# Performance work log

Hardware: AMD Instinct MI355X
Metric: run time of the kernel (lower is better)

Reference implementation:

```python
import jax, jax.numpy as jnp
import numpy as np

B, S, DIM = 4, 4096, 1024
H, HD = 16, 64  # n_heads, head_dim = dim // n_heads
UMV = 20.0      # unified_max_value (init kwarg)


def setup_inputs() -> dict:
    key = jax.random.key(0)
    kx, kw = jax.random.split(key)
    x = jax.random.normal(kx, (B, S, DIM), dtype=jnp.float32)
    # qkv_proj: Linear(dim, 3*dim). Small weight scale + positive bias keeps
    # attention scores inside the keep-window [0, 2*UMV] so denominators are safe.
    W_qkv = jax.random.normal(kw, (DIM, 3 * DIM), dtype=jnp.float32) * 0.02
    b_qkv = jnp.full((3 * DIM,), 0.5, dtype=jnp.float32)
    return {"x": x, "W_qkv": W_qkv, "b_qkv": b_qkv}


def reference(x, W_qkv, b_qkv):
    Bb, Ss, _ = x.shape
    qkv = x @ W_qkv + b_qkv                      # [B,S,3*dim]
    qkv = qkv.reshape(Bb, Ss, H, 3 * HD)          # [B,S,H,3*hd]
    Q, K, V = jnp.split(qkv, 3, axis=-1)          # each [B,S,H,hd]
    # matmul(Q, K.transpose(-2,-1)) on [B,S,H,hd]: contract head_dim -> [B,S,H,H]
    s = jnp.einsum('bshd,bsgd->bshg', Q, K) - UMV
    e = jnp.exp(s)
    mask = (s > UMV) | (s < -UMV)                 # keep only s in [-UMV, UMV]
    e = jnp.where(mask, 0.0, e)
    denom = jnp.sum(e, axis=-1, keepdims=True)
    p = e / denom                                  # [B,S,H,H]
    out = jnp.einsum('bshg,bsgd->bshd', p, V)      # [B,S,H,hd]
    return out
```

## Files before the change

### kernel.cpp

```cpp
#include <hip/hip_runtime.h>

typedef _Float16 v8h __attribute__((ext_vector_type(8)));
typedef _Float16 v4h __attribute__((ext_vector_type(4)));
typedef float v4f __attribute__((ext_vector_type(4)));

__device__ __forceinline__ void gl16(const void* g, void* l) {
    __builtin_amdgcn_global_load_lds(
        (const __attribute__((address_space(1))) unsigned int*)g,
        (__attribute__((address_space(3))) unsigned int*)l, 16, 0, 0);
}

__global__ __launch_bounds__(256) void k_cvt_x(const float* __restrict__ x,
                                               _Float16* __restrict__ x16) {
    int i = (blockIdx.x * 256 + threadIdx.x) * 8;
    float4 a = *(const float4*)(x + i);
    float4 b = *(const float4*)(x + i + 4);
    v8h h;
    h[0] = (_Float16)a.x; h[1] = (_Float16)a.y; h[2] = (_Float16)a.z; h[3] = (_Float16)a.w;
    h[4] = (_Float16)b.x; h[5] = (_Float16)b.y; h[6] = (_Float16)b.z; h[7] = (_Float16)b.w;
    *(v8h*)(x16 + i) = h;
}

__global__ __launch_bounds__(256) void k_cvt_w(const float* __restrict__ W,
                                               _Float16* __restrict__ Wt) {
    __shared__ float T[64][68];
    int k0 = (blockIdx.x & 15) * 64;
    int n0 = (blockIdx.x >> 4) * 64;
    int t = threadIdx.x;
    int tr = t >> 4;
    int tc = t & 15;
#pragma unroll
    for (int rr = 0; rr < 4; rr++) {
        int kk = rr * 16 + tr;
        float4 v = *(const float4*)(W + (size_t)(k0 + kk) * 3072 + n0 + tc * 4);
        T[kk][tc * 4 + 0] = v.x; T[kk][tc * 4 + 1] = v.y;
        T[kk][tc * 4 + 2] = v.z; T[kk][tc * 4 + 3] = v.w;
    }
    __syncthreads();
#pragma unroll
    for (int ww = 0; ww < 4; ww++) {
        int nn = ww * 16 + tr;
        v4h h;
#pragma unroll
        for (int i = 0; i < 4; i++) h[i] = (_Float16)T[tc * 4 + i][nn];
        *(v4h*)(Wt + (size_t)(n0 + nn) * 1024 + k0 + tc * 4) = h;
    }
}

__global__ __launch_bounds__(256) void k_gemm(const _Float16* __restrict__ A,
                                              const _Float16* __restrict__ Bt,
                                              const float* __restrict__ bias,
                                              float* __restrict__ C) {
    __shared__ __align__(16) _Float16 As[128 * 32];
    __shared__ __align__(16) _Float16 Bs[128 * 32];
    int bm = blockIdx.x & 127;
    int bn = blockIdx.x >> 7;
    int m0 = bm * 128, n0 = bn * 128;
    int tid = threadIdx.x;
    int w = tid >> 6, lane = tid & 63;
    int quad = lane >> 4, l15 = lane & 15;
    int wm = (w & 1) * 64, wn = (w >> 1) * 64;

    int mc1 = w * 16 + (lane >> 2);
    int mc2 = (w + 4) * 16 + (lane >> 2);
    int k8 = (lane & 3) * 8;
    const _Float16* aS1 = A + (size_t)(m0 + mc1) * 1024 + k8;
    const _Float16* aS2 = A + (size_t)(m0 + mc2) * 1024 + k8;
    const _Float16* bS1 = Bt + (size_t)(n0 + mc1) * 1024 + k8;
    const _Float16* bS2 = Bt + (size_t)(n0 + mc2) * 1024 + k8;
    _Float16* lA1 = &As[w * 512];
    _Float16* lA2 = &As[(w + 4) * 512];
    _Float16* lB1 = &Bs[w * 512];
    _Float16* lB2 = &Bs[(w + 4) * 512];

    v4f acc[4][4] = {};

    for (int kt = 0; kt < 1024; kt += 32) {
        __syncthreads();
        gl16(aS1 + kt, lA1);
        gl16(aS2 + kt, lA2);
        gl16(bS1 + kt, lB1);
        gl16(bS2 + kt, lB2);
        __syncthreads();
        v8h af[4], bf[4];
#pragma unroll
        for (int mi = 0; mi < 4; mi++)
            af[mi] = *(const v8h*)&As[(wm + mi * 16 + l15) * 32 + quad * 8];
#pragma unroll
        for (int ni = 0; ni < 4; ni++)
            bf[ni] = *(const v8h*)&Bs[(wn + ni * 16 + l15) * 32 + quad * 8];
#pragma unroll
        for (int mi = 0; mi < 4; mi++)
#pragma unroll
            for (int ni = 0; ni < 4; ni++)
                acc[mi][ni] = __builtin_amdgcn_mfma_f32_16x16x32_f16(af[mi], bf[ni], acc[mi][ni], 0, 0, 0);
    }

#pragma unroll
    for (int ni = 0; ni < 4; ni++) {
        int n = n0 + wn + ni * 16 + l15;
        float bv = bias[n];
#pragma unroll
        for (int mi = 0; mi < 4; mi++) {
            int mbase = m0 + wm + mi * 16 + quad * 4;
#pragma unroll
            for (int r = 0; r < 4; r++)
                C[(size_t)(mbase + r) * 3072 + n] = acc[mi][ni][r] + bv;
        }
    }
}

__global__ __launch_bounds__(256) void k_attn(const float* __restrict__ qkv,
                                              float* __restrict__ out) {
    __shared__ __align__(16) float lds[4 * 3408];
    int tid = threadIdx.x;
    int w = tid >> 6, lane = tid & 63;
    int pos = blockIdx.x * 4 + w;
    float* L = &lds[w * 3408];
    float* P = L + 3136;
    const float* src = qkv + (size_t)pos * 3072;

#pragma unroll
    for (int ii = 0; ii < 12; ii++) {
        int e = (ii * 64 + lane) * 4;
        float4 v = *(const float4*)(src + e);
        int h = e / 192, r = e % 192;
        *(float4*)(L + h * 196 + r) = v;
    }
    __syncthreads();

    {
        int h = lane & 15, quad = lane >> 4;
        const float* Qr = L + h * 196;
        const float* Kr0 = L + (quad * 4 + 0) * 196 + 64;
        const float* Kr1 = L + (quad * 4 + 1) * 196 + 64;
        const float* Kr2 = L + (quad * 4 + 2) * 196 + 64;
        const float* Kr3 = L + (quad * 4 + 3) * 196 + 64;
        float a0 = 0.f, a1 = 0.f, a2 = 0.f, a3 = 0.f;
#pragma unroll
        for (int d4 = 0; d4 < 16; d4++) {
            float4 q = *(const float4*)(Qr + d4 * 4);
            float4 k0 = *(const float4*)(Kr0 + d4 * 4);
            float4 k1 = *(const float4*)(Kr1 + d4 * 4);
            float4 k2 = *(const float4*)(Kr2 + d4 * 4);
            float4 k3 = *(const float4*)(Kr3 + d4 * 4);
            a0 += q.x * k0.x + q.y * k0.y + q.z * k0.z + q.w * k0.w;
            a1 += q.x * k1.x + q.y * k1.y + q.z * k1.z + q.w * k1.w;
            a2 += q.x * k2.x + q.y * k2.y + q.z * k2.z + q.w * k2.w;
            a3 += q.x * k3.x + q.y * k3.y + q.z * k3.z + q.w * k3.w;
        }
        float s0 = a0 - 20.0f, s1 = a1 - 20.0f, s2 = a2 - 20.0f, s3 = a3 - 20.0f;
        float e0 = (s0 > 20.0f || s0 < -20.0f) ? 0.0f : expf(s0);
        float e1 = (s1 > 20.0f || s1 < -20.0f) ? 0.0f : expf(s1);
        float e2 = (s2 > 20.0f || s2 < -20.0f) ? 0.0f : expf(s2);
        float e3 = (s3 > 20.0f || s3 < -20.0f) ? 0.0f : expf(s3);
        float part = e0 + e1 + e2 + e3;
        part += __shfl_xor(part, 16, 64);
        part += __shfl_xor(part, 32, 64);
        float inv = 1.0f / part;
        P[h * 17 + quad * 4 + 0] = e0 * inv;
        P[h * 17 + quad * 4 + 1] = e1 * inv;
        P[h * 17 + quad * 4 + 2] = e2 * inv;
        P[h * 17 + quad * 4 + 3] = e3 * inv;
    }
    __syncthreads();

    {
        int h2 = lane >> 2, db = (lane & 3) * 16;
        float o[16];
#pragma unroll
        for (int i = 0; i < 16; i++) o[i] = 0.f;
#pragma unroll
        for (int g = 0; g < 16; g++) {
            float p = P[h2 * 17 + g];
            const float* Vr = L + g * 196 + 128 + db;
#pragma unroll
            for (int d4 = 0; d4 < 4; d4++) {
                float4 v = *(const float4*)(Vr + d4 * 4);
                o[d4 * 4 + 0] += p * v.x;
                o[d4 * 4 + 1] += p * v.y;
                o[d4 * 4 + 2] += p * v.z;
                o[d4 * 4 + 3] += p * v.w;
            }
        }
        float* dst = out + (size_t)pos * 1024 + h2 * 64 + db;
#pragma unroll
        for (int d4 = 0; d4 < 4; d4++) {
            float4 v;
            v.x = o[d4 * 4 + 0]; v.y = o[d4 * 4 + 1];
            v.z = o[d4 * 4 + 2]; v.w = o[d4 * 4 + 3];
            *(float4*)(dst + d4 * 4) = v;
        }
    }
}

extern "C" void kernel_launch(void* const* d_in, const int* in_sizes, int n_in,
                              void* d_out, int out_size, void* d_ws, size_t ws_size,
                              hipStream_t stream) {
    (void)in_sizes; (void)n_in; (void)out_size; (void)ws_size;
    const float* x    = (const float*)d_in[0];
    const float* Wq   = (const float*)d_in[1];
    const float* bq   = (const float*)d_in[2];
    float* out = (float*)d_out;

    char* ws = (char*)d_ws;
    _Float16* x16  = (_Float16*)ws;
    _Float16* wt16 = (_Float16*)(ws + 33554432);
    float*    qkv  = (float*)(ws + 33554432 + 6291456);

    k_cvt_x<<<8192, 256, 0, stream>>>(x, x16);
    k_cvt_w<<<768, 256, 0, stream>>>(Wq, wt16);
    k_gemm<<<3072, 256, 0, stream>>>(x16, wt16, bq, qkv);
    k_attn<<<4096, 256, 0, stream>>>(qkv, out);
}
```

Baseline: 315.7 us.

## Store QKV intermediate in fp16 and use fdot2 in attention

```diff
diff --git a/kernel.cpp b/kernel.cpp
--- a/kernel.cpp
+++ b/kernel.cpp
@@ -2,6 +2,7 @@
 
 typedef _Float16 v8h __attribute__((ext_vector_type(8)));
 typedef _Float16 v4h __attribute__((ext_vector_type(4)));
+typedef _Float16 v2h __attribute__((ext_vector_type(2)));
 typedef float v4f __attribute__((ext_vector_type(4)));
 
 __device__ __forceinline__ void gl16(const void* g, void* l) {
@@ -50,7 +51,7 @@
 __global__ __launch_bounds__(256) void k_gemm(const _Float16* __restrict__ A,
                                               const _Float16* __restrict__ Bt,
                                               const float* __restrict__ bias,
-                                              float* __restrict__ C) {
+                                              _Float16* __restrict__ C) {
     __shared__ __align__(16) _Float16 As[128 * 32];
     __shared__ __align__(16) _Float16 Bs[128 * 32];
     int bm = blockIdx.x & 127;
@@ -105,63 +106,58 @@
             int mbase = m0 + wm + mi * 16 + quad * 4;
 #pragma unroll
             for (int r = 0; r < 4; r++)
-                C[(size_t)(mbase + r) * 3072 + n] = acc[mi][ni][r] + bv;
-        }
-    }
-}
-
-__global__ __launch_bounds__(256) void k_attn(const float* __restrict__ qkv,
+                C[(size_t)(mbase + r) * 3072 + n] = (_Float16)(acc[mi][ni][r] + bv);
+        }
+    }
+}
+
+__global__ __launch_bounds__(256) void k_attn(const _Float16* __restrict__ qkv,
                                               float* __restrict__ out) {
-    __shared__ __align__(16) float lds[4 * 3408];
+    __shared__ __align__(16) _Float16 Lh[4][16 * 200];
+    __shared__ float Pb[4][16 * 17];
     int tid = threadIdx.x;
     int w = tid >> 6, lane = tid & 63;
     int pos = blockIdx.x * 4 + w;
-    float* L = &lds[w * 3408];
-    float* P = L + 3136;
-    const float* src = qkv + (size_t)pos * 3072;
-
-#pragma unroll
-    for (int ii = 0; ii < 12; ii++) {
-        int e = (ii * 64 + lane) * 4;
-        float4 v = *(const float4*)(src + e);
+    _Float16* L = Lh[w];
+    float* P = Pb[w];
+    const _Float16* src = qkv + (size_t)pos * 3072;
+
+#pragma unroll
+    for (int ii = 0; ii < 6; ii++) {
+        int e = (ii * 64 + lane) * 8;
+        v8h v = *(const v8h*)(src + e);
         int h = e / 192, r = e % 192;
-        *(float4*)(L + h * 196 + r) = v;
+        *(v8h*)(L + h * 200 + r) = v;
     }
     __syncthreads();
 
     {
         int h = lane & 15, quad = lane >> 4;
-        const float* Qr = L + h * 196;
-        const float* Kr0 = L + (quad * 4 + 0) * 196 + 64;
-        const float* Kr1 = L + (quad * 4 + 1) * 196 + 64;
-        const float* Kr2 = L + (quad * 4 + 2) * 196 + 64;
-        const float* Kr3 = L + (quad * 4 + 3) * 196 + 64;
-        float a0 = 0.f, a1 = 0.f, a2 = 0.f, a3 = 0.f;
-#pragma unroll
-        for (int d4 = 0; d4 < 16; d4++) {
-            float4 q = *(const float4*)(Qr + d4 * 4);
-            float4 k0 = *(const float4*)(Kr0 + d4 * 4);
-            float4 k1 = *(const float4*)(Kr1 + d4 * 4);
-            float4 k2 = *(const float4*)(Kr2 + d4 * 4);
-            float4 k3 = *(const float4*)(Kr3 + d4 * 4);
-            a0 += q.x * k0.x + q.y * k0.y + q.z * k0.z + q.w * k0.w;
-            a1 += q.x * k1.x + q.y * k1.y + q.z * k1.z + q.w * k1.w;
-            a2 += q.x * k2.x + q.y * k2.y + q.z * k2.z + q.w * k2.w;
-            a3 += q.x * k3.x + q.y * k3.y + q.z * k3.z + q.w * k3.w;
-        }
-        float s0 = a0 - 20.0f, s1 = a1 - 20.0f, s2 = a2 - 20.0f, s3 = a3 - 20.0f;
-        float e0 = (s0 > 20.0f || s0 < -20.0f) ? 0.0f : expf(s0);
-        float e1 = (s1 > 20.0f || s1 < -20.0f) ? 0.0f : expf(s1);
-        float e2 = (s2 > 20.0f || s2 < -20.0f) ? 0.0f : expf(s2);
-        float e3 = (s3 > 20.0f || s3 < -20.0f) ? 0.0f : expf(s3);
-        float part = e0 + e1 + e2 + e3;
+        const _Float16* Qr = L + h * 200;
+        v8h q[8];
+#pragma unroll
+        for (int d = 0; d < 8; d++) q[d] = *(const v8h*)(Qr + d * 8);
+        float e4[4];
+#pragma unroll
+        for (int c = 0; c < 4; c++) {
+            const _Float16* Kr = L + (quad * 4 + c) * 200 + 64;
+            float a = 0.f;
+#pragma unroll
+            for (int d = 0; d < 8; d++) {
+                v8h k = *(const v8h*)(Kr + d * 8);
+#pragma unroll
+                for (int j = 0; j < 4; j++)
+                    a = __builtin_amdgcn_fdot2(((v2h*)&q[d])[j], ((v2h*)&k)[j], a, false);
+            }
+            float s = a - 20.0f;
+            e4[c] = (s > 20.0f || s < -20.0f) ? 0.0f : __expf(s);
+        }
+        float part = e4[0] + e4[1] + e4[2] + e4[3];
         part += __shfl_xor(part, 16, 64);
         part += __shfl_xor(part, 32, 64);
         float inv = 1.0f / part;
-        P[h * 17 + quad * 4 + 0] = e0 * inv;
-        P[h * 17 + quad * 4 + 1] = e1 * inv;
-        P[h * 17 + quad * 4 + 2] = e2 * inv;
-        P[h * 17 + quad * 4 + 3] = e3 * inv;
+#pragma unroll
+        for (int c = 0; c < 4; c++) P[h * 17 + quad * 4 + c] = e4[c] * inv;
     }
     __syncthreads();
 
@@ -173,14 +169,13 @@
 #pragma unroll
         for (int g = 0; g < 16; g++) {
             float p = P[h2 * 17 + g];
-            const float* Vr = L + g * 196 + 128 + db;
-#pragma unroll
-            for (int d4 = 0; d4 < 4; d4++) {
-                float4 v = *(const float4*)(Vr + d4 * 4);
-                o[d4 * 4 + 0] += p * v.x;
-                o[d4 * 4 + 1] += p * v.y;
-                o[d4 * 4 + 2] += p * v.z;
-                o[d4 * 4 + 3] += p * v.w;
+            const _Float16* Vr = L + g * 200 + 128 + db;
+            v8h v0 = *(const v8h*)(Vr);
+            v8h v1 = *(const v8h*)(Vr + 8);
+#pragma unroll
+            for (int i = 0; i < 8; i++) {
+                o[i]     += p * (float)v0[i];
+                o[8 + i] += p * (float)v1[i];
             }
         }
         float* dst = out + (size_t)pos * 1024 + h2 * 64 + db;
@@ -198,18 +193,18 @@
                               void* d_out, int out_size, void* d_ws, size_t ws_size,
                               hipStream_t stream) {
     (void)in_sizes; (void)n_in; (void)out_size; (void)ws_size;
-    const float* x    = (const float*)d_in[0];
-    const float* Wq   = (const float*)d_in[1];
-    const float* bq   = (const float*)d_in[2];
+    const float* x  = (const float*)d_in[0];
+    const float* Wq = (const float*)d_in[1];
+    const float* bq = (const float*)d_in[2];
     float* out = (float*)d_out;
 
     char* ws = (char*)d_ws;
-    _Float16* x16  = (_Float16*)ws;
-    _Float16* wt16 = (_Float16*)(ws + 33554432);
-    float*    qkv  = (float*)(ws + 33554432 + 6291456);
+    _Float16* x16   = (_Float16*)ws;
+    _Float16* wt16  = (_Float16*)(ws + (32u << 20));
+    _Float16* qkv16 = (_Float16*)(ws + (38u << 20));
 
     k_cvt_x<<<8192, 256, 0, stream>>>(x, x16);
     k_cvt_w<<<768, 256, 0, stream>>>(Wq, wt16);
-    k_gemm<<<3072, 256, 0, stream>>>(x16, wt16, bq, qkv);
-    k_attn<<<4096, 256, 0, stream>>>(qkv, out);
-}
+    k_gemm<<<3072, 256, 0, stream>>>(x16, wt16, bq, qkv16);
+    k_attn<<<4096, 256, 0, stream>>>(qkv16, out);
+}
```

After: 283.8 us. 10.1% less time.
